# Performance work log

Measured on AMD Instinct MI355X. Metric: run time of the kernel, lower is better.

The kernel has to match this reference:

```python
import jax, jax.numpy as jnp
import numpy as np
import math

B, L, D_NODE, D_PAIR, E = 4, 256, 256, 128, 65536
M0, M1 = 32, 8              # multiplicities of 0e and 1o node irreps
D_IRR = M0 + 3 * M1         # 56
WNUM = M0*M0 + M0*M1 + M1*M1 + M1*M0 + M1*M1  # 1664 per-edge TP weights
LN_EPS = 1e-5

# real-basis Wigner 3j for (1o x 2e -> 1o), e3nn conventions (l=1 order x,y,z;
# l=2 order xz, xy, (3y^2-r^2)-like, yz, (z^2-x^2)-like), normalized so sum(c^2)=1

def _w3j_121():
    s3 = 1.0 / math.sqrt(3.0)
    c = np.zeros((3, 5, 3), dtype=np.float32)  # [m1, m2, m3]
    X, Y, Z = 0, 1, 2
    c[X, 0, Z] = s3; c[Z, 0, X] = s3
    c[X, 1, Y] = s3; c[Y, 1, X] = s3
    c[X, 2, X] = -1.0/3.0; c[Y, 2, Y] = 2.0/3.0; c[Z, 2, Z] = -1.0/3.0
    c[Y, 3, Z] = s3; c[Z, 3, Y] = s3
    c[X, 4, X] = -s3; c[Z, 4, Z] = s3
    return jnp.asarray(c * math.sqrt(3.0 / 10.0))

W3J121 = _w3j_121()
# e3nn path weights: irrep_normalization='component', path_normalization='element'
PW0 = math.sqrt(1.0 / 40.0)   # paths -> 32x0e (fan 32+8)
PW1 = 0.25                    # paths -> 8x1o  (sqrt(3/48))
S3 = 1.0 / math.sqrt(3.0)     # w3j(0,1,1)=w3j(1,0,1)=w3j(1,1,0)=I/sqrt(3)


def _tensor_product(x, sh, w):
    # x: [E,56] = 32x0e + 8x1o (mul-major), sh: [E,9] = 0e+1o+2e, w: [E,1664]
    e = x.shape[0]
    x0 = x[:, :M0]                      # [E,32]
    x1 = x[:, M0:].reshape(e, M1, 3)    # [E,8,3]
    sh0, sh1, sh2 = sh[:, 0], sh[:, 1:4], sh[:, 4:9]
    W1 = w[:, :1024].reshape(e, M0, M0)       # 0e x 0e -> 0e
    W2 = w[:, 1024:1280].reshape(e, M0, M1)   # 0e x 1o -> 1o
    W3 = w[:, 1280:1344].reshape(e, M1, M1)   # 1o x 0e -> 1o
    W4 = w[:, 1344:1600].reshape(e, M1, M0)   # 1o x 1o -> 0e
    W5 = w[:, 1600:1664].reshape(e, M1, M1)   # 1o x 2e -> 1o
    out0 = PW0 * (jnp.einsum('eu,euw->ew', x0 * sh0[:, None], W1)
                  + S3 * jnp.einsum('eum,em,euw->ew', x1, sh1, W4))
    t5 = jnp.einsum('eua,abm,eb->eum', x1, W3J121, sh2)
    out1 = PW1 * (S3 * jnp.einsum('eu,em,euw->ewm', x0, sh1, W2)
                  + S3 * jnp.einsum('eum,euw->ewm', x1 * sh0[:, None, None], W3)
                  + jnp.einsum('eum,euw->ewm', t5, W5))
    return jnp.concatenate([out0, out1.reshape(e, 3 * M1)], axis=-1)  # [E,56]


def _fc(x, ln_g, ln_b, fc1_w, fc1_b, fc2_w, fc2_b):
    mu = jnp.mean(x, axis=-1, keepdims=True)
    var = jnp.mean(jnp.square(x - mu), axis=-1, keepdims=True)
    h = (x - mu) / jnp.sqrt(var + LN_EPS) * ln_g + ln_b
    h = jax.nn.relu(h @ fc1_w + fc1_b)   # dropout is identity at inference
    return h @ fc2_w + fc2_b             # [E,1664]


def reference(node, pair, l1_feats, edge_sh, proj_l0_w, proj_l0_b, proj_node_w, proj_node_b, ln_g, ln_b, fc1_w, fc1_b, fc2_w, fc2_b, pair_index, edge_src, edge_dst):
    n = B * L
    l0 = node @ proj_l0_w + proj_l0_b                              # [B,L,32]
    feats = jnp.concatenate([l0, l1_feats], axis=-1).reshape(n, D_IRR)
    b, i, j = pair_index
    edge_feats = pair[b, i, j]                                     # [E,128]
    w = _fc(edge_feats, ln_g, ln_b, fc1_w, fc1_b, fc2_w, fc2_b)
    conv = _tensor_product(feats[edge_dst], edge_sh, w)            # [E,56]
    sums = jax.ops.segment_sum(conv, edge_src, num_segments=n)
    cnt = jax.ops.segment_sum(jnp.ones((E,), conv.dtype), edge_src, num_segments=n)
    out = (sums / jnp.maximum(cnt, 1.0)[:, None]).reshape(B, L, D_IRR)
    l1_new = out[..., M0:] + l1_feats
    node_new = out[..., :M0] @ proj_node_w + proj_node_b + node
    return node_new, l1_new


def setup_inputs() -> dict:
    key = jax.random.key(0)
    ks = jax.random.split(key, 16)
    node = jax.random.normal(ks[0], (B, L, D_NODE), jnp.float32)
    pair = jax.random.normal(ks[1], (B, L, L, D_PAIR), jnp.float32)
    l1_feats = jax.random.normal(ks[2], (B, L, 3 * M1), jnp.float32)
    eb = jax.random.randint(ks[3], (E,), 0, B)
    ei = jax.random.randint(ks[4], (E,), 0, L)
    ej = jax.random.randint(ks[5], (E,), 0, L)
    pair_index = jnp.stack([eb, ei, ej]).astype(jnp.int32)
    edge_src = (eb * L + ei).astype(jnp.int32)
    edge_dst = (eb * L + ej).astype(jnp.int32)
    edge_sh = jax.random.normal(ks[6], (E, 9), jnp.float32)
    return {
        'node': node, 'pair': pair, 'l1_feats': l1_feats, 'edge_sh': edge_sh,
        'proj_l0_w': jax.random.normal(ks[7], (D_NODE, M0), jnp.float32) / math.sqrt(D_NODE),
        'proj_l0_b': 0.1 * jax.random.normal(ks[8], (M0,), jnp.float32),
        'proj_node_w': jax.random.normal(ks[9], (M0, D_NODE), jnp.float32) / math.sqrt(M0),
        'proj_node_b': 0.1 * jax.random.normal(ks[10], (D_NODE,), jnp.float32),
        'ln_g': jnp.ones((D_PAIR,), jnp.float32),
        'ln_b': jnp.zeros((D_PAIR,), jnp.float32),
        'fc1_w': jax.random.normal(ks[11], (D_PAIR, D_PAIR), jnp.float32) / math.sqrt(D_PAIR),
        'fc1_b': 0.1 * jax.random.normal(ks[12], (D_PAIR,), jnp.float32),
        'fc2_w': jax.random.normal(ks[13], (D_PAIR, WNUM), jnp.float32) / math.sqrt(D_PAIR),
        'fc2_b': 0.1 * jax.random.normal(ks[14], (WNUM,), jnp.float32),
        'pair_index': pair_index, 'edge_src': edge_src, 'edge_dst': edge_dst,
    }
```

## Files before the change

### kernel.cpp

```cpp
#include <hip/hip_runtime.h>

#define LQ 256
#define EDGES 65536
#define NNODE 1024
#define ET 64
#define NT 512
#define WSTR 66

typedef __attribute__((ext_vector_type(8))) short bf16x8;
typedef __attribute__((ext_vector_type(4))) float f32x4;
typedef unsigned short ushort_t;
typedef unsigned int uint32;

constexpr float PW0c = 0.15811388300841897f;
constexpr float PW1c = 0.25f;
constexpr float S3c  = 0.57735026918962576f;
constexpr float Kc   = 0.54772255750516611f;

__device__ __forceinline__ ushort_t f2bf(float x){
  unsigned u = __float_as_uint(x);
  unsigned r = u + 0x7FFFu + ((u >> 16) & 1u);
  return (ushort_t)(r >> 16);
}

__device__ __forceinline__ float red8(float v){
  v += __shfl_xor(v, 1);
  v += __shfl_xor(v, 2);
  v += __shfl_xor(v, 4);
  return v;
}

__global__ __launch_bounds__(512) void prep_kernel(
    const float* __restrict__ fc1w, const float* __restrict__ fc2w,
    ushort_t* __restrict__ fc1wT, ushort_t* __restrict__ fc2wT)
{
  const int i = blockIdx.x*512 + threadIdx.x;
  if (i < 16384){
    const int j = i >> 7, k = i & 127;
    fc1wT[i] = f2bf(fc1w[k*128 + j]);
  } else {
    const int i2 = i - 16384;
    const int j = i2 >> 7, k = i2 & 127;
    fc2wT[i2] = f2bf(fc2w[(size_t)k*1664 + j]);
  }
}

__global__ __launch_bounds__(64) void feats_kernel(
    const float* __restrict__ node, const float* __restrict__ l1,
    const float* __restrict__ w, const float* __restrict__ b,
    float* __restrict__ feats)
{
  const int rr = blockIdx.x;
  const int t = threadIdx.x;
  if (t < 32){
    float acc = b[t];
    const float* nr = node + rr*256;
    #pragma unroll 4
    for (int c=0;c<256;c++) acc += nr[c]*w[c*32+t];
    feats[rr*64+t] = acc;
  } else if (t < 56){
    feats[rr*64+t] = l1[rr*24 + (t-32)];
  }
}

__global__ __launch_bounds__(256) void count_kernel(
    const int* __restrict__ src, float* __restrict__ cnt)
{
  const int ee = blockIdx.x*256 + threadIdx.x;
  atomicAdd(&cnt[src[ee]], 1.0f);
}

__global__ __launch_bounds__(NT) void edge_kernel(
    const float* __restrict__ pair, const int* __restrict__ pidx,
    const int* __restrict__ esrc, const int* __restrict__ edst,
    const float* __restrict__ esh,
    const float* __restrict__ lng, const float* __restrict__ lnb,
    const ushort_t* __restrict__ fc1wT, const float* __restrict__ fc1b,
    const ushort_t* __restrict__ fc2wT, const float* __restrict__ fc2b,
    const float* __restrict__ feats, float* __restrict__ sums)
{
  __shared__ float sWch[128*WSTR];
  __shared__ unsigned char sH[64*256];
  __shared__ unsigned char sBt[128*256];
  __shared__ float sC[ET*129];
  __shared__ int s_src[ET], s_dst[ET];

  const int t = threadIdx.x;
  const int e0g = blockIdx.x * ET;
  unsigned char* xnb = (unsigned char*)sWch;

  if (t < ET){ s_src[t] = esrc[e0g+t]; s_dst[t] = edst[e0g+t]; }

  const uint4* gW1 = (const uint4*)fc1wT;
  const uint4* gW2 = (const uint4*)fc2wT;
  uint4 pfA[4], pfB[4];
  #pragma unroll
  for (int u=0;u<4;u++) pfA[u] = gW1[u*NT + t];

  __syncthreads();

  const int e = t >> 3;
  const int r = t & 7;

  {
    const float* f = feats + (size_t)s_dst[e]*64;
    const float* sh = esh + (size_t)(e0g+e)*9;
    const float sh0 = sh[0], s1x = sh[1], s1y = sh[2], s1z = sh[3];
    float* C = sC + e*129;
    #pragma unroll
    for (int q=0;q<4;q++){
      const int u = r*4+q;
      const float x0u = f[u];
      C[u]    = PW0c*sh0*x0u;
      C[40+u] = PW1c*S3c*x0u;
    }
    {
      const int u = r;
      const float xx = f[32+u*3+0], xy = f[32+u*3+1], xz = f[32+u*3+2];
      C[32+u] = PW0c*S3c*(xx*s1x + xy*s1y + xz*s1z);
      const float bc = PW1c*S3c*sh0;
      C[72+u*3+0] = bc*xx; C[72+u*3+1] = bc*xy; C[72+u*3+2] = bc*xz;
      const float s20=sh[4], s21=sh[5], s22=sh[6], s23=sh[7], s24=sh[8];
      const float RXX = Kc*(-(1.f/3.f)*s22 - S3c*s24);
      const float RXY = Kc*S3c*s21;
      const float RXZ = Kc*S3c*s20;
      const float RYY = Kc*((2.f/3.f)*s22);
      const float RYZ = Kc*S3c*s23;
      const float RZZ = Kc*(-(1.f/3.f)*s22 + S3c*s24);
      C[96+u*3+0] = PW1c*(xx*RXX + xy*RXY + xz*RXZ);
      C[96+u*3+1] = PW1c*(xx*RXY + xy*RYY + xz*RYZ);
      C[96+u*3+2] = PW1c*(xx*RXZ + xy*RYZ + xz*RZZ);
      if (r==0){ C[120]=s1x; C[121]=s1y; C[122]=s1z; }
    }
  }

  {
    const int ee = e0g + e;
    const int pb = pidx[ee], pi_ = pidx[EDGES+ee], pj = pidx[2*EDGES+ee];
    const float4* prow = (const float4*)(pair + (((size_t)pb*LQ + pi_)*LQ + pj)*128);
    float4 v[4];
    #pragma unroll
    for (int k=0;k<4;k++) v[k] = prow[r*4+k];
    float s=0.f, s2=0.f;
    #pragma unroll
    for (int k=0;k<4;k++){
      s  += v[k].x+v[k].y+v[k].z+v[k].w;
      s2 += v[k].x*v[k].x + v[k].y*v[k].y + v[k].z*v[k].z + v[k].w*v[k].w;
    }
    s = red8(s); s2 = red8(s2);
    const float mean = s * (1.f/128.f);
    const float var  = s2 * (1.f/128.f) - mean*mean;
    const float rstd = rsqrtf(var + 1e-5f);
    uint32 pk[8];
    #pragma unroll
    for (int k=0;k<4;k++){
      const int c = r*16 + k*4;
      const float4 g  = *(const float4*)(lng + c);
      const float4 bb = *(const float4*)(lnb + c);
      float4 o;
      o.x = (v[k].x-mean)*rstd*g.x + bb.x;
      o.y = (v[k].y-mean)*rstd*g.y + bb.y;
      o.z = (v[k].z-mean)*rstd*g.z + bb.z;
      o.w = (v[k].w-mean)*rstd*g.w + bb.w;
      pk[k*2]   = (uint32)f2bf(o.x) | ((uint32)f2bf(o.y)<<16);
      pk[k*2+1] = (uint32)f2bf(o.z) | ((uint32)f2bf(o.w)<<16);
    }
    const int xr = (e&7)<<4;
    *(uint4*)(xnb + e*256 + ((r*32) ^ xr))      = make_uint4(pk[0],pk[1],pk[2],pk[3]);
    *(uint4*)(xnb + e*256 + ((r*32+16) ^ xr))   = make_uint4(pk[4],pk[5],pk[6],pk[7]);
  }

  #pragma unroll
  for (int u=0;u<4;u++){
    const int v = u*NT + t; const int n = v>>4; const int c = v&15;
    *(uint4*)(sBt + n*256 + ((c*16) ^ ((n&7)<<4))) = pfA[u];
  }
  #pragma unroll
  for (int u=0;u<4;u++) pfB[u] = gW2[u*NT + t];
  __syncthreads();

  const int l = t & 63;
  const int l15 = l & 15;
  const int lh = l >> 4;
  const int wv = t >> 6;
  const int mt0 = (wv & 1) * 2;
  const int npr = wv >> 1;
  const int erow0 = mt0*16 + l15;
  const int ax = (l15 & 7) << 4;
  const int jc0 = npr*32 + l15;
  const int bx = ax;
  const int ebase = mt0*16 + lh*4;

  {
    const float bj0 = fc1b[jc0], bj1 = fc1b[jc0+16];
    f32x4 acc00 = {bj0,bj0,bj0,bj0}, acc01 = {bj1,bj1,bj1,bj1};
    f32x4 acc10 = acc00, acc11 = acc01;
    #pragma unroll
    for (int kk=0;kk<4;kk++){
      const int ko = kk*64 + lh*16;
      bf16x8 a0 = *(const bf16x8*)(xnb + erow0*256 + (ko ^ ax));
      bf16x8 a1 = *(const bf16x8*)(xnb + (erow0+16)*256 + (ko ^ ax));
      bf16x8 b0 = *(const bf16x8*)(sBt + jc0*256 + (ko ^ bx));
      bf16x8 b1 = *(const bf16x8*)(sBt + (jc0+16)*256 + (ko ^ bx));
      acc00 = __builtin_amdgcn_mfma_f32_16x16x32_bf16(a0,b0,acc00,0,0,0);
      acc01 = __builtin_amdgcn_mfma_f32_16x16x32_bf16(a0,b1,acc01,0,0,0);
      acc10 = __builtin_amdgcn_mfma_f32_16x16x32_bf16(a1,b0,acc10,0,0,0);
      acc11 = __builtin_amdgcn_mfma_f32_16x16x32_bf16(a1,b1,acc11,0,0,0);
    }
    #pragma unroll
    for (int q=0;q<4;q++){
      const int ea = ebase + q, eb = ea + 16;
      *(ushort_t*)(sH + ea*256 + ((jc0*2) ^ ((ea&7)<<4)))      = f2bf(fmaxf(acc00[q],0.f));
      *(ushort_t*)(sH + ea*256 + (((jc0+16)*2) ^ ((ea&7)<<4))) = f2bf(fmaxf(acc01[q],0.f));
      *(ushort_t*)(sH + eb*256 + ((jc0*2) ^ ((eb&7)<<4)))      = f2bf(fmaxf(acc10[q],0.f));
      *(ushort_t*)(sH + eb*256 + (((jc0+16)*2) ^ ((eb&7)<<4))) = f2bf(fmaxf(acc11[q],0.f));
    }
  }
  __syncthreads();

  float o0[4] = {0.f,0.f,0.f,0.f};
  float o1[3] = {0.f,0.f,0.f};
  const float* Ca = sC + e*129;

#define APPLY(CB) do {                                                        \
    if ((CB) < 8){                                                            \
      const int u0 = (CB)*4;                                                  \
      _Pragma("unroll")                                                       \
      for (int q=0;q<4;q++){                                                  \
        const int wi = r*4+q;                                                 \
        float sacc = 0.f;                                                     \
        _Pragma("unroll")                                                     \
        for (int du=0;du<4;du++)                                              \
          sacc += Ca[u0+du]*sWch[(du*32+wi)*WSTR+e];                          \
        o0[q] += sacc;                                                        \
      }                                                                       \
    } else if ((CB) < 10){                                                    \
      const int u0 = ((CB)-8)*16;                                             \
      float S = 0.f;                                                          \
      _Pragma("unroll")                                                       \
      for (int du=0;du<16;du++)                                               \
        S += Ca[40+u0+du]*sWch[(du*8+r)*WSTR+e];                              \
      o1[0] += S*Ca[120]; o1[1] += S*Ca[121]; o1[2] += S*Ca[122];             \
    } else if ((CB) == 10){                                                   \
      _Pragma("unroll")                                                       \
      for (int u=0;u<8;u++){                                                  \
        const float wvv = sWch[(u*8+r)*WSTR+e];                               \
        o1[0] += Ca[72+u*3+0]*wvv;                                            \
        o1[1] += Ca[72+u*3+1]*wvv;                                            \
        o1[2] += Ca[72+u*3+2]*wvv;                                            \
      }                                                                       \
      _Pragma("unroll")                                                       \
      for (int q=0;q<4;q++){                                                  \
        const int wi = r*4+q;                                                 \
        o0[q] += Ca[32]*sWch[(64+wi)*WSTR+e] + Ca[33]*sWch[(96+wi)*WSTR+e];   \
      }                                                                       \
    } else if ((CB) == 11){                                                   \
      _Pragma("unroll")                                                       \
      for (int q=0;q<4;q++){                                                  \
        const int wi = r*4+q;                                                 \
        _Pragma("unroll")                                                     \
        for (int du=0;du<4;du++)                                              \
          o0[q] += Ca[34+du]*sWch[(du*32+wi)*WSTR+e];                         \
      }                                                                       \
    } else {                                                                  \
      _Pragma("unroll")                                                       \
      for (int q=0;q<4;q++){                                                  \
        const int wi = r*4+q;                                                 \
        o0[q] += Ca[38]*sWch[wi*WSTR+e] + Ca[39]*sWch[(32+wi)*WSTR+e];        \
      }                                                                       \
      _Pragma("unroll")                                                       \
      for (int u=0;u<8;u++){                                                  \
        const float wvv = sWch[(64+u*8+r)*WSTR+e];                            \
        o1[0] += Ca[96+u*3+0]*wvv;                                            \
        o1[1] += Ca[96+u*3+1]*wvv;                                            \
        o1[2] += Ca[96+u*3+2]*wvv;                                            \
      }                                                                       \
    }                                                                         \
  } while(0)

#define CHUNK(CB, CUR, NXT, DOLOAD) do {                                      \
    _Pragma("unroll")                                                         \
    for (int u=0;u<4;u++){                                                    \
      const int v = u*NT + t; const int n = v>>4; const int c = v&15;         \
      *(uint4*)(sBt + n*256 + ((c*16) ^ ((n&7)<<4))) = CUR[u];                \
    }                                                                         \
    if (DOLOAD){                                                              \
      _Pragma("unroll")                                                       \
      for (int u=0;u<4;u++) NXT[u] = gW2[((CB)+1)*2048 + u*NT + t];           \
    }                                                                         \
    __syncthreads();                                                          \
    {                                                                         \
      const float bj0 = fc2b[(CB)*128 + jc0];                                 \
      const float bj1 = fc2b[(CB)*128 + jc0 + 16];                            \
      f32x4 acc00 = {bj0,bj0,bj0,bj0}, acc01 = {bj1,bj1,bj1,bj1};             \
      f32x4 acc10 = acc00, acc11 = acc01;                                     \
      _Pragma("unroll")                                                       \
      for (int kk=0;kk<4;kk++){                                               \
        const int ko = kk*64 + lh*16;                                         \
        bf16x8 a0 = *(const bf16x8*)(sH + erow0*256 + (ko ^ ax));             \
        bf16x8 a1 = *(const bf16x8*)(sH + (erow0+16)*256 + (ko ^ ax));        \
        bf16x8 b0 = *(const bf16x8*)(sBt + jc0*256 + (ko ^ bx));              \
        bf16x8 b1 = *(const bf16x8*)(sBt + (jc0+16)*256 + (ko ^ bx));         \
        acc00 = __builtin_amdgcn_mfma_f32_16x16x32_bf16(a0,b0,acc00,0,0,0);   \
        acc01 = __builtin_amdgcn_mfma_f32_16x16x32_bf16(a0,b1,acc01,0,0,0);   \
        acc10 = __builtin_amdgcn_mfma_f32_16x16x32_bf16(a1,b0,acc10,0,0,0);   \
        acc11 = __builtin_amdgcn_mfma_f32_16x16x32_bf16(a1,b1,acc11,0,0,0);   \
      }                                                                       \
      _Pragma("unroll")                                                       \
      for (int q=0;q<4;q++){                                                  \
        sWch[jc0*WSTR + ebase + q]           = acc00[q];                      \
        sWch[(jc0+16)*WSTR + ebase + q]      = acc01[q];                      \
        sWch[jc0*WSTR + ebase + 16 + q]      = acc10[q];                      \
        sWch[(jc0+16)*WSTR + ebase + 16 + q] = acc11[q];                      \
      }                                                                       \
    }                                                                         \
    __syncthreads();                                                          \
    APPLY(CB);                                                                \
    __syncthreads();                                                          \
  } while(0)

  CHUNK(0,  pfB, pfA, 1);
  CHUNK(1,  pfA, pfB, 1);
  CHUNK(2,  pfB, pfA, 1);
  CHUNK(3,  pfA, pfB, 1);
  CHUNK(4,  pfB, pfA, 1);
  CHUNK(5,  pfA, pfB, 1);
  CHUNK(6,  pfB, pfA, 1);
  CHUNK(7,  pfA, pfB, 1);
  CHUNK(8,  pfB, pfA, 1);
  CHUNK(9,  pfA, pfB, 1);
  CHUNK(10, pfB, pfA, 1);
  CHUNK(11, pfA, pfB, 1);
  CHUNK(12, pfB, pfA, 0);

  float* srow = sums + (size_t)s_src[e]*64;
  #pragma unroll
  for (int q=0;q<4;q++) atomicAdd(srow + r*4 + q, o0[q]);
  #pragma unroll
  for (int m=0;m<3;m++) atomicAdd(srow + 32 + r*3 + m, o1[m]);
}

__global__ __launch_bounds__(256) void finalize_kernel(
    const float* __restrict__ sums, const float* __restrict__ cnt,
    const float* __restrict__ node, const float* __restrict__ l1,
    const float* __restrict__ pw, const float* __restrict__ pb,
    float* __restrict__ out)
{
  __shared__ float so[56];
  const int rnode = blockIdx.x;
  const int t = threadIdx.x;
  if (t < 56){
    const float c = cnt[rnode];
    so[t] = sums[rnode*64+t] / fmaxf(c, 1.0f);
  }
  __syncthreads();
  float acc = pb[t] + node[rnode*256+t];
  #pragma unroll
  for (int k=0;k<32;k++) acc += so[k]*pw[k*256+t];
  out[rnode*256+t] = acc;
  if (t < 24) out[NNODE*256 + rnode*24 + t] = so[32+t] + l1[rnode*24+t];
}

extern "C" void kernel_launch(void* const* d_in, const int* in_sizes, int n_in,
                              void* d_out, int out_size, void* d_ws, size_t ws_size,
                              hipStream_t stream)
{
  const float* node = (const float*)d_in[0];
  const float* pair = (const float*)d_in[1];
  const float* l1f  = (const float*)d_in[2];
  const float* esh  = (const float*)d_in[3];
  const float* plw  = (const float*)d_in[4];
  const float* plb  = (const float*)d_in[5];
  const float* pnw  = (const float*)d_in[6];
  const float* pnb  = (const float*)d_in[7];
  const float* lng  = (const float*)d_in[8];
  const float* lnb  = (const float*)d_in[9];
  const float* fc1w = (const float*)d_in[10];
  const float* fc1b = (const float*)d_in[11];
  const float* fc2w = (const float*)d_in[12];
  const float* fc2b = (const float*)d_in[13];
  const int* pidx = (const int*)d_in[14];
  const int* esrc = (const int*)d_in[15];
  const int* edst = (const int*)d_in[16];
  float* out = (float*)d_out;
  float* ws = (float*)d_ws;
  float* feats = ws;
  float* sums  = ws + 65536;
  float* cnt   = ws + 131072;
  ushort_t* fc1wT = (ushort_t*)(ws + 132096);
  ushort_t* fc2wT = fc1wT + 16384;

  hipMemsetAsync(sums, 0, (65536+1024)*sizeof(float), stream);
  prep_kernel<<<dim3(448), dim3(512), 0, stream>>>(fc1w, fc2w, fc1wT, fc2wT);
  feats_kernel<<<dim3(1024), dim3(64), 0, stream>>>(node, l1f, plw, plb, feats);
  count_kernel<<<dim3(256), dim3(256), 0, stream>>>(esrc, cnt);
  edge_kernel<<<dim3(1024), dim3(NT), 0, stream>>>(pair, pidx, esrc, edst, esh,
      lng, lnb, fc1wT, fc1b, fc2wT, fc2b, feats, sums);
  finalize_kernel<<<dim3(1024), dim3(256), 0, stream>>>(sums, cnt, node, l1f, pnw, pnb, out);
}
```

Measured before the change: 442.0 us.

## Shrink edge kernel LDS, move coefficients to registers, merge setup kernels

Merges the prep, feats and count kernels into a single setup launch to cut launch overhead. The edge kernel reuses three aliased LDS regions (about 80KB in place of roughly 137KB) and adds launch_bounds(…,4) so more blocks can be resident per CU. Per-edge TP coefficients now sit in registers and are broadcast with shuffles. The weight chunk is stored as swizzled f32x4 vector writes, and staging of the next B tile is folded into the apply phase, dropping one barrier per chunk. The trade-offs are extra shuffle work and register pressure under the tighter launch bound, which may cause spills.

```diff
diff --git a/kernel.cpp b/kernel.cpp
--- a/kernel.cpp
+++ b/kernel.cpp
@@ -5,7 +5,6 @@
 #define NNODE 1024
 #define ET 64
 #define NT 512
-#define WSTR 66
 
 typedef __attribute__((ext_vector_type(8))) short bf16x8;
 typedef __attribute__((ext_vector_type(4))) float f32x4;
@@ -30,47 +29,44 @@
   return v;
 }
 
-__global__ __launch_bounds__(512) void prep_kernel(
+__global__ __launch_bounds__(512) void setup_kernel(
     const float* __restrict__ fc1w, const float* __restrict__ fc2w,
-    ushort_t* __restrict__ fc1wT, ushort_t* __restrict__ fc2wT)
+    ushort_t* __restrict__ fc1wT, ushort_t* __restrict__ fc2wT,
+    const float* __restrict__ node, const float* __restrict__ l1,
+    const float* __restrict__ plw, const float* __restrict__ plb,
+    float* __restrict__ feats,
+    const int* __restrict__ esrc, float* __restrict__ cnt)
 {
-  const int i = blockIdx.x*512 + threadIdx.x;
-  if (i < 16384){
-    const int j = i >> 7, k = i & 127;
-    fc1wT[i] = f2bf(fc1w[k*128 + j]);
+  const int b = blockIdx.x, t = threadIdx.x;
+  if (b < 448){
+    const int i = b*512 + t;
+    if (i < 16384){
+      const int j = i >> 7, k = i & 127;
+      fc1wT[i] = f2bf(fc1w[k*128 + j]);
+    } else {
+      const int i2 = i - 16384;
+      const int j = i2 >> 7, k = i2 & 127;
+      fc2wT[i2] = f2bf(fc2w[(size_t)k*1664 + j]);
+    }
+  } else if (b < 576){
+    const int rr = (b-448)*8 + (t >> 6);
+    const int u = t & 63;
+    if (u < 32){
+      float acc = plb[u];
+      const float* nr = node + rr*256;
+      #pragma unroll 4
+      for (int c=0;c<256;c++) acc += nr[c]*plw[c*32+u];
+      feats[rr*64+u] = acc;
+    } else if (u < 56){
+      feats[rr*64+u] = l1[rr*24 + (u-32)];
+    }
   } else {
-    const int i2 = i - 16384;
-    const int j = i2 >> 7, k = i2 & 127;
-    fc2wT[i2] = f2bf(fc2w[(size_t)k*1664 + j]);
-  }
-}
-
-__global__ __launch_bounds__(64) void feats_kernel(
-    const float* __restrict__ node, const float* __restrict__ l1,
-    const float* __restrict__ w, const float* __restrict__ b,
-    float* __restrict__ feats)
-{
-  const int rr = blockIdx.x;
-  const int t = threadIdx.x;
-  if (t < 32){
-    float acc = b[t];
-    const float* nr = node + rr*256;
-    #pragma unroll 4
-    for (int c=0;c<256;c++) acc += nr[c]*w[c*32+t];
-    feats[rr*64+t] = acc;
-  } else if (t < 56){
-    feats[rr*64+t] = l1[rr*24 + (t-32)];
-  }
-}
-
-__global__ __launch_bounds__(256) void count_kernel(
-    const int* __restrict__ src, float* __restrict__ cnt)
-{
-  const int ee = blockIdx.x*256 + threadIdx.x;
-  atomicAdd(&cnt[src[ee]], 1.0f);
-}
-
-__global__ __launch_bounds__(NT) void edge_kernel(
+    const int ee = (b-576)*512 + t;
+    atomicAdd(&cnt[esrc[ee]], 1.0f);
+  }
+}
+
+__global__ __launch_bounds__(NT, 4) void edge_kernel(
     const float* __restrict__ pair, const int* __restrict__ pidx,
     const int* __restrict__ esrc, const int* __restrict__ edst,
     const float* __restrict__ esh,
@@ -79,34 +75,27 @@
     const ushort_t* __restrict__ fc2wT, const float* __restrict__ fc2b,
     const float* __restrict__ feats, float* __restrict__ sums)
 {
-  __shared__ float sWch[128*WSTR];
-  __shared__ unsigned char sH[64*256];
-  __shared__ unsigned char sBt[128*256];
-  __shared__ float sC[ET*129];
-  __shared__ int s_src[ET], s_dst[ET];
+  __shared__ unsigned char R1[32768];
+  __shared__ unsigned char R2[32768];
+  __shared__ unsigned char R3[16384];
 
   const int t = threadIdx.x;
   const int e0g = blockIdx.x * ET;
-  unsigned char* xnb = (unsigned char*)sWch;
-
-  if (t < ET){ s_src[t] = esrc[e0g+t]; s_dst[t] = edst[e0g+t]; }
+  const int e = t >> 3;
+  const int r = t & 7;
 
   const uint4* gW1 = (const uint4*)fc1wT;
   const uint4* gW2 = (const uint4*)fc2wT;
-  uint4 pfA[4], pfB[4];
-  #pragma unroll
-  for (int u=0;u<4;u++) pfA[u] = gW1[u*NT + t];
-
-  __syncthreads();
-
-  const int e = t >> 3;
-  const int r = t & 7;
+  uint4 pf[4];
+  #pragma unroll
+  for (int u=0;u<4;u++) pf[u] = gW1[u*NT + t];
 
   {
-    const float* f = feats + (size_t)s_dst[e]*64;
+    const int dst = edst[e0g + e];
+    const float* f = feats + (size_t)dst*64;
     const float* sh = esh + (size_t)(e0g+e)*9;
     const float sh0 = sh[0], s1x = sh[1], s1y = sh[2], s1z = sh[3];
-    float* C = sC + e*129;
+    float* C = (float*)(R1 + e*512);
     #pragma unroll
     for (int q=0;q<4;q++){
       const int u = r*4+q;
@@ -133,6 +122,19 @@
       if (r==0){ C[120]=s1x; C[121]=s1y; C[122]=s1z; }
     }
   }
+  __syncthreads();
+
+  float cr[16];
+  {
+    const unsigned char* cp = R1 + e*512 + r*64;
+    *(float4*)&cr[0]  = *(const float4*)(cp);
+    *(float4*)&cr[4]  = *(const float4*)(cp+16);
+    *(float4*)&cr[8]  = *(const float4*)(cp+32);
+    *(float4*)&cr[12] = *(const float4*)(cp+48);
+  }
+  __syncthreads();
+
+#define CF(I) __shfl(cr[(I)&15], (t & 56) + ((I)>>4))
 
   {
     const int ee = e0g + e;
@@ -166,17 +168,17 @@
       pk[k*2+1] = (uint32)f2bf(o.z) | ((uint32)f2bf(o.w)<<16);
     }
     const int xr = (e&7)<<4;
-    *(uint4*)(xnb + e*256 + ((r*32) ^ xr))      = make_uint4(pk[0],pk[1],pk[2],pk[3]);
-    *(uint4*)(xnb + e*256 + ((r*32+16) ^ xr))   = make_uint4(pk[4],pk[5],pk[6],pk[7]);
+    *(uint4*)(R1 + e*256 + ((r*32) ^ xr))    = make_uint4(pk[0],pk[1],pk[2],pk[3]);
+    *(uint4*)(R1 + e*256 + ((r*32+16) ^ xr)) = make_uint4(pk[4],pk[5],pk[6],pk[7]);
   }
 
   #pragma unroll
   for (int u=0;u<4;u++){
     const int v = u*NT + t; const int n = v>>4; const int c = v&15;
-    *(uint4*)(sBt + n*256 + ((c*16) ^ ((n&7)<<4))) = pfA[u];
-  }
-  #pragma unroll
-  for (int u=0;u<4;u++) pfB[u] = gW2[u*NT + t];
+    *(uint4*)(R2 + n*256 + ((c*16) ^ ((n&7)<<4))) = pf[u];
+  }
+  #pragma unroll
+  for (int u=0;u<4;u++) pf[u] = gW2[u*NT + t];
   __syncthreads();
 
   const int l = t & 63;
@@ -188,8 +190,8 @@
   const int erow0 = mt0*16 + l15;
   const int ax = (l15 & 7) << 4;
   const int jc0 = npr*32 + l15;
-  const int bx = ax;
   const int ebase = mt0*16 + lh*4;
+  const int e4 = e*4;
 
   {
     const float bj0 = fc1b[jc0], bj1 = fc1b[jc0+16];
@@ -198,10 +200,10 @@
     #pragma unroll
     for (int kk=0;kk<4;kk++){
       const int ko = kk*64 + lh*16;
-      bf16x8 a0 = *(const bf16x8*)(xnb + erow0*256 + (ko ^ ax));
-      bf16x8 a1 = *(const bf16x8*)(xnb + (erow0+16)*256 + (ko ^ ax));
-      bf16x8 b0 = *(const bf16x8*)(sBt + jc0*256 + (ko ^ bx));
-      bf16x8 b1 = *(const bf16x8*)(sBt + (jc0+16)*256 + (ko ^ bx));
+      bf16x8 a0 = *(const bf16x8*)(R1 + erow0*256 + (ko ^ ax));
+      bf16x8 a1 = *(const bf16x8*)(R1 + (erow0+16)*256 + (ko ^ ax));
+      bf16x8 b0 = *(const bf16x8*)(R2 + jc0*256 + (ko ^ ax));
+      bf16x8 b1 = *(const bf16x8*)(R2 + (jc0+16)*256 + (ko ^ ax));
       acc00 = __builtin_amdgcn_mfma_f32_16x16x32_bf16(a0,b0,acc00,0,0,0);
       acc01 = __builtin_amdgcn_mfma_f32_16x16x32_bf16(a0,b1,acc01,0,0,0);
       acc10 = __builtin_amdgcn_mfma_f32_16x16x32_bf16(a1,b0,acc10,0,0,0);
@@ -210,85 +212,82 @@
     #pragma unroll
     for (int q=0;q<4;q++){
       const int ea = ebase + q, eb = ea + 16;
-      *(ushort_t*)(sH + ea*256 + ((jc0*2) ^ ((ea&7)<<4)))      = f2bf(fmaxf(acc00[q],0.f));
-      *(ushort_t*)(sH + ea*256 + (((jc0+16)*2) ^ ((ea&7)<<4))) = f2bf(fmaxf(acc01[q],0.f));
-      *(ushort_t*)(sH + eb*256 + ((jc0*2) ^ ((eb&7)<<4)))      = f2bf(fmaxf(acc10[q],0.f));
-      *(ushort_t*)(sH + eb*256 + (((jc0+16)*2) ^ ((eb&7)<<4))) = f2bf(fmaxf(acc11[q],0.f));
-    }
-  }
-  __syncthreads();
+      *(ushort_t*)(R3 + ea*256 + ((jc0*2) ^ ((ea&7)<<4)))      = f2bf(fmaxf(acc00[q],0.f));
+      *(ushort_t*)(R3 + ea*256 + (((jc0+16)*2) ^ ((ea&7)<<4))) = f2bf(fmaxf(acc01[q],0.f));
+      *(ushort_t*)(R3 + eb*256 + ((jc0*2) ^ ((eb&7)<<4)))      = f2bf(fmaxf(acc10[q],0.f));
+      *(ushort_t*)(R3 + eb*256 + (((jc0+16)*2) ^ ((eb&7)<<4))) = f2bf(fmaxf(acc11[q],0.f));
+    }
+  }
+  __syncthreads();
+
+  #pragma unroll
+  for (int u=0;u<4;u++){
+    const int v = u*NT + t; const int n = v>>4; const int c = v&15;
+    *(uint4*)(R2 + n*256 + ((c*16) ^ ((n&7)<<4))) = pf[u];
+  }
+  #pragma unroll
+  for (int u=0;u<4;u++) pf[u] = gW2[2048 + u*NT + t];
 
   float o0[4] = {0.f,0.f,0.f,0.f};
   float o1[3] = {0.f,0.f,0.f};
-  const float* Ca = sC + e*129;
+
+#define WVX(ROW) (*(const float*)(R1 + (ROW)*256 + (e4 ^ (((ROW)&7)<<4))))
 
 #define APPLY(CB) do {                                                        \
     if ((CB) < 8){                                                            \
       const int u0 = (CB)*4;                                                  \
+      const float k0=CF(u0), k1=CF(u0+1), k2=CF(u0+2), k3=CF(u0+3);           \
       _Pragma("unroll")                                                       \
       for (int q=0;q<4;q++){                                                  \
         const int wi = r*4+q;                                                 \
-        float sacc = 0.f;                                                     \
-        _Pragma("unroll")                                                     \
-        for (int du=0;du<4;du++)                                              \
-          sacc += Ca[u0+du]*sWch[(du*32+wi)*WSTR+e];                          \
-        o0[q] += sacc;                                                        \
+        o0[q] += k0*WVX(wi) + k1*WVX(32+wi) + k2*WVX(64+wi) + k3*WVX(96+wi);  \
       }                                                                       \
     } else if ((CB) < 10){                                                    \
       const int u0 = ((CB)-8)*16;                                             \
       float S = 0.f;                                                          \
       _Pragma("unroll")                                                       \
       for (int du=0;du<16;du++)                                               \
-        S += Ca[40+u0+du]*sWch[(du*8+r)*WSTR+e];                              \
-      o1[0] += S*Ca[120]; o1[1] += S*Ca[121]; o1[2] += S*Ca[122];             \
+        S += CF(40+u0+du)*WVX(du*8+r);                                        \
+      o1[0] += S*CF(120); o1[1] += S*CF(121); o1[2] += S*CF(122);             \
     } else if ((CB) == 10){                                                   \
       _Pragma("unroll")                                                       \
       for (int u=0;u<8;u++){                                                  \
-        const float wvv = sWch[(u*8+r)*WSTR+e];                               \
-        o1[0] += Ca[72+u*3+0]*wvv;                                            \
-        o1[1] += Ca[72+u*3+1]*wvv;                                            \
-        o1[2] += Ca[72+u*3+2]*wvv;                                            \
+        const float wvv = WVX(u*8+r);                                         \
+        o1[0] += CF(72+u*3+0)*wvv;                                            \
+        o1[1] += CF(72+u*3+1)*wvv;                                            \
+        o1[2] += CF(72+u*3+2)*wvv;                                            \
       }                                                                       \
       _Pragma("unroll")                                                       \
       for (int q=0;q<4;q++){                                                  \
         const int wi = r*4+q;                                                 \
-        o0[q] += Ca[32]*sWch[(64+wi)*WSTR+e] + Ca[33]*sWch[(96+wi)*WSTR+e];   \
+        o0[q] += CF(32)*WVX(64+wi) + CF(33)*WVX(96+wi);                       \
       }                                                                       \
     } else if ((CB) == 11){                                                   \
+      const float k0=CF(34), k1=CF(35), k2=CF(36), k3=CF(37);                 \
       _Pragma("unroll")                                                       \
       for (int q=0;q<4;q++){                                                  \
         const int wi = r*4+q;                                                 \
-        _Pragma("unroll")                                                     \
-        for (int du=0;du<4;du++)                                              \
-          o0[q] += Ca[34+du]*sWch[(du*32+wi)*WSTR+e];                         \
+        o0[q] += k0*WVX(wi) + k1*WVX(32+wi) + k2*WVX(64+wi) + k3*WVX(96+wi);  \
       }                                                                       \
     } else {                                                                  \
+      const float k0=CF(38), k1=CF(39);                                       \
       _Pragma("unroll")                                                       \
       for (int q=0;q<4;q++){                                                  \
         const int wi = r*4+q;                                                 \
-        o0[q] += Ca[38]*sWch[wi*WSTR+e] + Ca[39]*sWch[(32+wi)*WSTR+e];        \
+        o0[q] += k0*WVX(wi) + k1*WVX(32+wi);                                  \
       }                                                                       \
       _Pragma("unroll")                                                       \
       for (int u=0;u<8;u++){                                                  \
-        const float wvv = sWch[(64+u*8+r)*WSTR+e];                            \
-        o1[0] += Ca[96+u*3+0]*wvv;                                            \
-        o1[1] += Ca[96+u*3+1]*wvv;                                            \
-        o1[2] += Ca[96+u*3+2]*wvv;                                            \
+        const float wvv = WVX(64+u*8+r);                                      \
+        o1[0] += CF(96+u*3+0)*wvv;                                            \
+        o1[1] += CF(96+u*3+1)*wvv;                                            \
+        o1[2] += CF(96+u*3+2)*wvv;                                            \
       }                                                                       \
     }                                                                         \
   } while(0)
 
-#define CHUNK(CB, CUR, NXT, DOLOAD) do {                                      \
-    _Pragma("unroll")                                                         \
-    for (int u=0;u<4;u++){                                                    \
-      const int v = u*NT + t; const int n = v>>4; const int c = v&15;         \
-      *(uint4*)(sBt + n*256 + ((c*16) ^ ((n&7)<<4))) = CUR[u];                \
-    }                                                                         \
-    if (DOLOAD){                                                              \
-      _Pragma("unroll")                                                       \
-      for (int u=0;u<4;u++) NXT[u] = gW2[((CB)+1)*2048 + u*NT + t];           \
-    }                                                                         \
-    __syncthreads();                                                          \
+#define CHUNKM(CB, DO_STAGE, DO_LOAD) do {                                    \
+    __syncthreads();      \
     {                                                                         \
       const float bj0 = fc2b[(CB)*128 + jc0];                                 \
       const float bj1 = fc2b[(CB)*128 + jc0 + 16];                            \
@@ -297,43 +296,42 @@
       _Pragma("unroll")                                                       \
       for (int kk=0;kk<4;kk++){                                               \
         const int ko = kk*64 + lh*16;                                         \
-        bf16x8 a0 = *(const bf16x8*)(sH + erow0*256 + (ko ^ ax));             \
-        bf16x8 a1 = *(const bf16x8*)(sH + (erow0+16)*256 + (ko ^ ax));        \
-        bf16x8 b0 = *(const bf16x8*)(sBt + jc0*256 + (ko ^ bx));              \
-        bf16x8 b1 = *(const bf16x8*)(sBt + (jc0+16)*256 + (ko ^ bx));         \
+        bf16x8 a0 = *(const bf16x8*)(R3 + erow0*256 + (ko ^ ax));             \
+        bf16x8 a1 = *(const bf16x8*)(R3 + (erow0+16)*256 + (ko ^ ax));        \
+        bf16x8 b0 = *(const bf16x8*)(R2 + jc0*256 + (ko ^ ax));               \
+        bf16x8 b1 = *(const bf16x8*)(R2 + (jc0+16)*256 + (ko ^ ax));          \
         acc00 = __builtin_amdgcn_mfma_f32_16x16x32_bf16(a0,b0,acc00,0,0,0);   \
         acc01 = __builtin_amdgcn_mfma_f32_16x16x32_bf16(a0,b1,acc01,0,0,0);   \
         acc10 = __builtin_amdgcn_mfma_f32_16x16x32_bf16(a1,b0,acc10,0,0,0);   \
         acc11 = __builtin_amdgcn_mfma_f32_16x16x32_bf16(a1,b1,acc11,0,0,0);   \
       }                                                                       \
-      _Pragma("unroll")                                                       \
-      for (int q=0;q<4;q++){                                                  \
-        sWch[jc0*WSTR + ebase + q]           = acc00[q];                      \
-        sWch[(jc0+16)*WSTR + ebase + q]      = acc01[q];                      \
-        sWch[jc0*WSTR + ebase + 16 + q]      = acc10[q];                      \
-        sWch[(jc0+16)*WSTR + ebase + 16 + q] = acc11[q];                      \
-      }                                                                       \
+      *(f32x4*)(R1 + jc0*256      + ((ebase*4) ^ ax))      = acc00;           \
+      *(f32x4*)(R1 + (jc0+16)*256 + ((ebase*4) ^ ax))      = acc01;           \
+      *(f32x4*)(R1 + jc0*256      + (((ebase+16)*4) ^ ax)) = acc10;           \
+      *(f32x4*)(R1 + (jc0+16)*256 + (((ebase+16)*4) ^ ax)) = acc11;           \
     }                                                                         \
-    __syncthreads();                                                          \
+    __syncthreads();               \
     APPLY(CB);                                                                \
-    __syncthreads();                                                          \
+    if (DO_STAGE){                                                            \
+      _Pragma("unroll")                                                       \
+      for (int u=0;u<4;u++){                                                  \
+        const int v = u*NT + t; const int n = v>>4; const int c = v&15;       \
+        *(uint4*)(R2 + n*256 + ((c*16) ^ ((n&7)<<4))) = pf[u];                \
+      }                                                                       \
+      if (DO_LOAD){                                                           \
+        _Pragma("unroll")                                                     \
+        for (int u=0;u<4;u++) pf[u] = gW2[((CB)+2)*2048 + u*NT + t];          \
+      }                                                                       \
+    }                                                                         \
   } while(0)
 
-  CHUNK(0,  pfB, pfA, 1);
-  CHUNK(1,  pfA, pfB, 1);
-  CHUNK(2,  pfB, pfA, 1);
-  CHUNK(3,  pfA, pfB, 1);
-  CHUNK(4,  pfB, pfA, 1);
-  CHUNK(5,  pfA, pfB, 1);
-  CHUNK(6,  pfB, pfA, 1);
-  CHUNK(7,  pfA, pfB, 1);
-  CHUNK(8,  pfB, pfA, 1);
-  CHUNK(9,  pfA, pfB, 1);
-  CHUNK(10, pfB, pfA, 1);
-  CHUNK(11, pfA, pfB, 1);
-  CHUNK(12, pfB, pfA, 0);
-
-  float* srow = sums + (size_t)s_src[e]*64;
+  CHUNKM(0,1,1);  CHUNKM(1,1,1);  CHUNKM(2,1,1);  CHUNKM(3,1,1);
+  CHUNKM(4,1,1);  CHUNKM(5,1,1);  CHUNKM(6,1,1);  CHUNKM(7,1,1);
+  CHUNKM(8,1,1);  CHUNKM(9,1,1);  CHUNKM(10,1,1); CHUNKM(11,1,0);
+  CHUNKM(12,0,0);
+
+  const int src = esrc[e0g + e];
+  float* srow = sums + (size_t)src*64;
   #pragma unroll
   for (int q=0;q<4;q++) atomicAdd(srow + r*4 + q, o0[q]);
   #pragma unroll
@@ -391,9 +389,8 @@
   ushort_t* fc2wT = fc1wT + 16384;
 
   hipMemsetAsync(sums, 0, (65536+1024)*sizeof(float), stream);
-  prep_kernel<<<dim3(448), dim3(512), 0, stream>>>(fc1w, fc2w, fc1wT, fc2wT);
-  feats_kernel<<<dim3(1024), dim3(64), 0, stream>>>(node, l1f, plw, plb, feats);
-  count_kernel<<<dim3(256), dim3(256), 0, stream>>>(esrc, cnt);
+  setup_kernel<<<dim3(704), dim3(512), 0, stream>>>(fc1w, fc2w, fc1wT, fc2wT,
+      node, l1f, plw, plb, feats, esrc, cnt);
   edge_kernel<<<dim3(1024), dim3(NT), 0, stream>>>(pair, pidx, esrc, edst, esh,
       lng, lnb, fc1wT, fc1b, fc2wT, fc2b, feats, sums);
   finalize_kernel<<<dim3(1024), dim3(256), 0, stream>>>(sums, cnt, node, l1f, pnw, pnb, out);
```

After: 414.2 us. -6.3%, faster.
